# Performance work log

Measured on AMD Instinct MI355X. Metric: run time of the kernel, lower is better.

## Reference

```python
import jax, jax.numpy as jnp
import numpy as np

B, L1, L2 = 4, 1024, 512
D_PG, D_EX = 2304, 1024
H, HKV, DH = 8, 4, 256
SCALE = 256.0 ** -0.5


def _rope(x, cos, sin):
    # x: [B, L, h, DH]; cos/sin: [B, L, 1, DH//2]
    x = x.astype(jnp.float32)
    x1, x2 = jnp.split(x, 2, axis=-1)
    return jnp.concatenate([x1 * cos - x2 * sin, x2 * cos + x1 * sin], axis=-1)


def setup_inputs() -> dict:
    key = jax.random.key(0)
    ks = jax.random.split(key, 16)
    s = 0.02
    return {
        "pg_embeds": jax.random.normal(ks[0], (B, L1, D_PG), jnp.float32),
        "ex_embeds": jax.random.normal(ks[1], (B, L2, D_EX), jnp.float32),
        "cos": jax.random.normal(ks[2], (B, L1 + L2, 1, DH // 2), jnp.float32),
        "sin": jax.random.normal(ks[3], (B, L1 + L2, 1, DH // 2), jnp.float32),
        "attention_mask": jnp.zeros((B, L1 + L2, L1 + L2), jnp.float32),
        "Wq0": jax.random.normal(ks[4], (H * DH, D_PG), jnp.float32) * s,
        "Wk0": jax.random.normal(ks[5], (HKV * DH, D_PG), jnp.float32) * s,
        "Wv0": jax.random.normal(ks[6], (HKV * DH, D_PG), jnp.float32) * s,
        "Wo0": jax.random.normal(ks[7], (D_PG, H * DH), jnp.float32) * s,
        "Wq1": jax.random.normal(ks[8], (H * DH, D_EX), jnp.float32) * s,
        "Wk1": jax.random.normal(ks[9], (HKV * DH, D_EX), jnp.float32) * s,
        "Wv1": jax.random.normal(ks[10], (HKV * DH, D_EX), jnp.float32) * s,
        "Wo1": jax.random.normal(ks[11], (D_EX, H * DH), jnp.float32) * s,
    }


def reference(pg_embeds, ex_embeds, cos, sin, attention_mask,
              Wq0, Wk0, Wv0, Wo0, Wq1, Wk1, Wv1, Wo1):
    b, l1 = pg_embeds.shape[0], pg_embeds.shape[1]
    l2 = ex_embeds.shape[1]
    # per-stream QKV projections, then concat along sequence
    q = jnp.concatenate([
        (pg_embeds @ Wq0.T).reshape(b, l1, H, DH),
        (ex_embeds @ Wq1.T).reshape(b, l2, H, DH)], axis=1)
    k = jnp.concatenate([
        (pg_embeds @ Wk0.T).reshape(b, l1, HKV, DH),
        (ex_embeds @ Wk1.T).reshape(b, l2, HKV, DH)], axis=1)
    v = jnp.concatenate([
        (pg_embeds @ Wv0.T).reshape(b, l1, HKV, DH),
        (ex_embeds @ Wv1.T).reshape(b, l2, HKV, DH)], axis=1)
    q = _rope(q, cos, sin)  # fp32
    k = _rope(k, cos, sin)
    # GQA: repeat KV heads to match query heads
    rep = H // HKV
    k = jnp.repeat(k, rep, axis=2)
    v = jnp.repeat(jnp.repeat(v, rep, axis=2).astype(jnp.float32), 1, axis=0)
    # scores: [B, H, L, L]
    scores = jnp.einsum('bqhd,bkhd->bhqk', q, k) * SCALE
    scores = scores + attention_mask[:, None, :, :]
    p = jax.nn.softmax(scores, axis=-1)
    att = jnp.einsum('bhqk,bkhd->bqhd', p, v).reshape(b, l1 + l2, H * DH)
    out0 = att[:, :l1] @ Wo0.T
    out1 = att[:, l1:] @ Wo1.T
    return (out0, out1)
```

## Files before the change

### kernel.cpp

```cpp
#include <hip/hip_runtime.h>
#include <stdint.h>
#include <stddef.h>


typedef _Float16 f16;
typedef _Float16 f16x8 __attribute__((ext_vector_type(8)));
typedef _Float16 f16x4 __attribute__((ext_vector_type(4)));
typedef float    f32x4 __attribute__((ext_vector_type(4)));

__device__ __forceinline__ void async_ld16(const void* g, void* l) {
  __builtin_amdgcn_global_load_lds((const __attribute__((address_space(1))) void*)g,
                                   (__attribute__((address_space(3))) void*)l,
                                   16, 0, 0);
}

template <typename Epi>
__device__ __forceinline__ void gemm_core(f16* At, f16* Bt,
                                          const f16* __restrict__ A, int lda,
                                          const f16* __restrict__ Bm, int ldb,
                                          int K, Epi&& epi)
{
  const int t    = threadIdx.x;
  const int w    = t >> 6;
  const int lane = t & 63;
  const int q4   = lane >> 4;
  const int l16  = lane & 15;
  const int wm   = w >> 1;
  const int wn   = w & 1;

  const f32x4 vzero = {0.f, 0.f, 0.f, 0.f};
  f32x4 acc[4][4];
#pragma unroll
  for (int i = 0; i < 4; ++i)
#pragma unroll
    for (int j = 0; j < 4; ++j) acc[i][j] = vzero;

  const int srow = t >> 2;
  const int scol = (t & 3) << 3;
  const f16* aP = A  + (size_t)srow * lda + scol;
  const f16* bP = Bm + (size_t)srow * ldb + scol;
  f16* ldsA0 = At + w * 512;
  f16* ldsA1 = At + 2048 + w * 512;
  f16* ldsB0 = Bt + w * 512;
  f16* ldsB1 = Bt + 2048 + w * 512;
  const size_t a64 = (size_t)64 * lda;
  const size_t b64 = (size_t)64 * ldb;

  for (int k0 = 0; k0 < K; k0 += 32) {
    async_ld16(aP + k0,        ldsA0);
    async_ld16(aP + a64 + k0,  ldsA1);
    async_ld16(bP + k0,        ldsB0);
    async_ld16(bP + b64 + k0,  ldsB1);
    __syncthreads();

    f16x8 af[4], bf[4];
#pragma unroll
    for (int mi = 0; mi < 4; ++mi)
      af[mi] = *(const f16x8*)(At + (wm * 64 + mi * 16 + l16) * 32 + q4 * 8);
#pragma unroll
    for (int ni = 0; ni < 4; ++ni)
      bf[ni] = *(const f16x8*)(Bt + (wn * 64 + ni * 16 + l16) * 32 + q4 * 8);

#pragma unroll
    for (int mi = 0; mi < 4; ++mi)
#pragma unroll
      for (int ni = 0; ni < 4; ++ni)
        acc[mi][ni] = __builtin_amdgcn_mfma_f32_16x16x32_f16(af[mi], bf[ni], acc[mi][ni], 0, 0, 0);
    __syncthreads();
  }

#pragma unroll
  for (int mi = 0; mi < 4; ++mi)
#pragma unroll
    for (int ni = 0; ni < 4; ++ni)
#pragma unroll
      for (int r = 0; r < 4; ++r)
        epi(wm * 64 + mi * 16 + q4 * 4 + r, wn * 64 + ni * 16 + l16, acc[mi][ni][r]);
}

__global__ __launch_bounds__(256) void k_qkv(
    const f16* __restrict__ xpg, const f16* __restrict__ xex,
    const f16* __restrict__ W0,  const f16* __restrict__ W1,
    const float* __restrict__ cs, const float* __restrict__ sn,
    f16* __restrict__ q, f16* __restrict__ k, f16* __restrict__ v)
{
  __shared__ alignas(16) f16 At[128 * 32];
  __shared__ alignas(16) f16 Bt[128 * 32];
  const int idx = blockIdx.x;
  const bool s0 = idx < 1024;
  int by, bx, K;
  const f16 *A, *B;
  if (s0) { by = idx >> 5; bx = idx & 31; K = 2304;
            A = xpg + (size_t)by * 128 * 2304; B = W0 + (size_t)bx * 128 * 2304; }
  else    { int j = idx - 1024; by = j >> 5; bx = j & 31; K = 1024;
            A = xex + (size_t)by * 128 * 1024; B = W1 + (size_t)bx * 128 * 1024; }
  const int rowbase = by * 128, colbase = bx * 128;
  gemm_core(At, Bt, A, K, B, K, K, [&](int r, int c, float fv) {
    int m = rowbase + r;
    int row = s0 ? ((m >> 10) * 1536 + (m & 1023))
                 : ((m >> 9) * 1536 + 1024 + (m & 511));
    int col = colbase + c;
    float p = __shfl_xor(fv, 1, 64);
    if (col < 3072) {
      int j = (col & 255) >> 1;
      float cv = cs[(size_t)row * 128 + j];
      float sv = sn[(size_t)row * 128 + j];
      float y = (col & 1) ? (fv * cv + p * sv) : (fv * cv - p * sv);
      f16 h = (f16)y;
      if (col < 2048) q[(size_t)row * 2048 + col]        = h;
      else            k[(size_t)row * 1024 + col - 2048] = h;
    } else {
      v[(size_t)row * 1024 + col - 3072] = (f16)fv;
    }
  });
}

__global__ __launch_bounds__(256) void k_vtrans(const f16* __restrict__ v,
                                                f16* __restrict__ vt)
{
  __shared__ f16 tile[32][33];
  const int b = blockIdx.z;
  const int d0 = blockIdx.x * 32, l0 = blockIdx.y * 32;
  const int t = threadIdx.x;
  const int tr = t >> 5, tc = t & 31;
#pragma unroll
  for (int i = 0; i < 4; ++i) {
    int l = l0 + tr + i * 8;
    tile[tr + i * 8][tc] = v[((size_t)b * 1536 + l) * 1024 + d0 + tc];
  }
  __syncthreads();
#pragma unroll
  for (int i = 0; i < 4; ++i) {
    int d = d0 + tr + i * 8;
    int g = d >> 8, dw = d & 255;
    vt[(((size_t)b * 4 + g) * 256 + dw) * 1536 + l0 + tc] = tile[tc][tr + i * 8];
  }
}

__global__ __launch_bounds__(256) void k_attn(
    const f16* __restrict__ qb, const f16* __restrict__ kb,
    const f16* __restrict__ mask, f16* __restrict__ Sdst,
    const f16* __restrict__ Psrc, const f16* __restrict__ vt,
    f16* __restrict__ att0, f16* __restrict__ att1,
    int b_sc, int b_pv, int npv)
{
  __shared__ alignas(16) f16 At[128 * 32];
  __shared__ alignas(16) f16 Bt[128 * 32];
  const int idx = blockIdx.x;
  if (idx < npv) {
    const int h = idx / 24, rem = idx % 24, by = rem >> 1, bx = rem & 1;
    const f16* A = Psrc + (size_t)h * 1536 * 1536 + (size_t)by * 128 * 1536;
    const f16* B = vt + (size_t)(b_pv * 4 + (h >> 1)) * 256 * 1536 + (size_t)bx * 128 * 1536;
    const int rowbase = by * 128, colbase = bx * 128;
    gemm_core(At, Bt, A, 1536, B, 1536, 1536, [&](int r, int c, float fv) {
      int m = rowbase + r;
      if (m < 1024) att0[((size_t)(b_pv * 1024 + m))       * 2048 + h * 256 + colbase + c] = (f16)fv;
      else          att1[((size_t)(b_pv * 512 + m - 1024)) * 2048 + h * 256 + colbase + c] = (f16)fv;
    });
  } else {
    const int j = idx - npv;
    const int h = j / 144, rem = j % 144, by = rem / 12, bx = rem % 12;
    const f16* A = qb + (size_t)b_sc * 1536 * 2048 + h * 256 + (size_t)by * 128 * 2048;
    const f16* B = kb + (size_t)b_sc * 1536 * 1024 + (h >> 1) * 256 + (size_t)bx * 128 * 1024;
    f16* Sz = Sdst + (size_t)h * 1536 * 1536;
    const f16* mb = mask + (size_t)b_sc * 1536 * 1536;
    const int rowbase = by * 128, colbase = bx * 128;
    gemm_core(At, Bt, A, 2048, B, 1024, 256, [&](int r, int c, float fv) {
      size_t i = (size_t)(rowbase + r) * 1536 + colbase + c;
      Sz[i] = (f16)(fv * 0.0625f + (float)mb[i]);
    });
  }
}

__global__ __launch_bounds__(256) void k_softmax(f16* __restrict__ S)
{
  const int row = blockIdx.x * 4 + (threadIdx.x >> 6);
  const int lane = threadIdx.x & 63;
  f16* p = S + (size_t)row * 1536 + lane * 8;
  f16x8 v0 = *(const f16x8*)p;
  f16x8 v1 = *(const f16x8*)(p + 512);
  f16x8 v2 = *(const f16x8*)(p + 1024);
  float x[24];
#pragma unroll
  for (int i = 0; i < 8; ++i) {
    x[i] = (float)v0[i]; x[8 + i] = (float)v1[i]; x[16 + i] = (float)v2[i];
  }
  float mx = x[0];
#pragma unroll
  for (int i = 1; i < 24; ++i) mx = fmaxf(mx, x[i]);
#pragma unroll
  for (int o = 32; o > 0; o >>= 1) mx = fmaxf(mx, __shfl_xor(mx, o, 64));
  float s = 0.f;
#pragma unroll
  for (int i = 0; i < 24; ++i) { x[i] = __expf(x[i] - mx); s += x[i]; }
#pragma unroll
  for (int o = 32; o > 0; o >>= 1) s += __shfl_xor(s, o, 64);
  const float inv = 1.f / s;
  f16x8 o0, o1, o2;
#pragma unroll
  for (int i = 0; i < 8; ++i) {
    o0[i] = (f16)(x[i] * inv); o1[i] = (f16)(x[8 + i] * inv); o2[i] = (f16)(x[16 + i] * inv);
  }
  *(f16x8*)p = o0; *(f16x8*)(p + 512) = o1; *(f16x8*)(p + 1024) = o2;
}

__global__ __launch_bounds__(256) void k_tail(
    const f16* __restrict__ Psrc, const f16* __restrict__ vt,
    f16* __restrict__ att0, f16* __restrict__ att1,
    const f16* __restrict__ wo0, const f16* __restrict__ wo1,
    float* __restrict__ out0, float* __restrict__ out1)
{
  __shared__ alignas(16) f16 At[128 * 32];
  __shared__ alignas(16) f16 Bt[128 * 32];
  const int idx = blockIdx.x;
  if (idx < 192) {
    const int h = idx / 24, rem = idx % 24, by = rem >> 1, bx = rem & 1;
    const f16* A = Psrc + (size_t)h * 1536 * 1536 + (size_t)by * 128 * 1536;
    const f16* B = vt + (size_t)(3 * 4 + (h >> 1)) * 256 * 1536 + (size_t)bx * 128 * 1536;
    const int rowbase = by * 128, colbase = bx * 128;
    gemm_core(At, Bt, A, 1536, B, 1536, 1536, [&](int r, int c, float fv) {
      int m = rowbase + r;
      if (m < 1024) att0[((size_t)(3 * 1024 + m))       * 2048 + h * 256 + colbase + c] = (f16)fv;
      else          att1[((size_t)(3 * 512 + m - 1024)) * 2048 + h * 256 + colbase + c] = (f16)fv;
    });
  } else if (idx < 624) {
    const int j = idx - 192;
    const int by = j / 18, bx = j % 18;
    const f16* A = att0 + (size_t)by * 128 * 2048;
    const f16* B = wo0 + (size_t)bx * 128 * 2048;
    const int rowbase = by * 128, colbase = bx * 128;
    gemm_core(At, Bt, A, 2048, B, 2048, 2048, [&](int r, int c, float fv) {
      out0[(size_t)(rowbase + r) * 2304 + colbase + c] = fv;
    });
  } else {
    const int j = idx - 624;
    const int by = j >> 3, bx = j & 7;
    const f16* A = att1 + (size_t)by * 128 * 2048;
    const f16* B = wo1 + (size_t)bx * 128 * 2048;
    const int rowbase = by * 128, colbase = bx * 128;
    gemm_core(At, Bt, A, 2048, B, 2048, 2048, [&](int r, int c, float fv) {
      out1[(size_t)(rowbase + r) * 1024 + colbase + c] = fv;
    });
  }
}

__global__ __launch_bounds__(256) void k_oproj3(
    const f16* __restrict__ att0, const f16* __restrict__ att1,
    const f16* __restrict__ wo0,  const f16* __restrict__ wo1,
    float* __restrict__ out0, float* __restrict__ out1)
{
  __shared__ alignas(16) f16 At[128 * 32];
  __shared__ alignas(16) f16 Bt[128 * 32];
  const int idx = blockIdx.x;
  int by, bx, ldc;
  const f16 *A, *B;
  float* C;
  if (idx < 144) { by = 24 + idx / 18; bx = idx % 18;
                   A = att0 + (size_t)by * 128 * 2048; B = wo0 + (size_t)bx * 128 * 2048;
                   C = out0; ldc = 2304; }
  else           { int j = idx - 144; by = 12 + (j >> 3); bx = j & 7;
                   A = att1 + (size_t)by * 128 * 2048; B = wo1 + (size_t)bx * 128 * 2048;
                   C = out1; ldc = 1024; }
  const int rowbase = by * 128, colbase = bx * 128;
  gemm_core(At, Bt, A, 2048, B, 2048, 2048, [&](int r, int c, float fv) {
    C[(size_t)(rowbase + r) * ldc + colbase + c] = fv;
  });
}

__global__ __launch_bounds__(256) void k_cast_all(
    const float* __restrict__ s0, const float* __restrict__ s1,
    const float* __restrict__ s2, const float* __restrict__ s3,
    const float* __restrict__ s4, const float* __restrict__ s5,
    f16* __restrict__ ws)
{
  const size_t gid = ((size_t)blockIdx.x * 256 + threadIdx.x) * 4;
  const float* s; size_t off, dst;
  if      (gid < 9437184ull)  { s = s0; off = gid;               dst = 0ull        + off; }
  else if (gid < 11534336ull) { s = s1; off = gid - 9437184ull;  dst = 9437184ull  + off; }
  else if (gid < 13893632ull) { s = s2; off = gid - 11534336ull; dst = 18612224ull + off; }
  else if (gid < 18612224ull) { s = s3; off = gid - 13893632ull; dst = 20971520ull + off; }
  else if (gid < 19660800ull) { s = s4; off = gid - 18612224ull; dst = 28835840ull + off; }
  else                        { s = s5; off = gid - 19660800ull; dst = 29884416ull + off; }
  float4 v = *(const float4*)(s + off);
  f16x4 o = {(f16)v.x, (f16)v.y, (f16)v.z, (f16)v.w};
  *(f16x4*)(ws + dst) = o;
}

__global__ __launch_bounds__(256) void k_cast_wr(
    const float* __restrict__ wq0, const float* __restrict__ wk0,
    const float* __restrict__ wq1, const float* __restrict__ wk1,
    f16* __restrict__ W0c, f16* __restrict__ W1c)
{
  const int idx = blockIdx.x;
  const float* src; f16* dstm; int K, r, drow;
  if      (idx < 2048) { src = wq0; dstm = W0c; K = 2304; r = idx;        drow = idx; }
  else if (idx < 3072) { src = wk0; dstm = W0c; K = 2304; r = idx - 2048; drow = idx; }
  else if (idx < 5120) { src = wq1; dstm = W1c; K = 1024; r = idx - 3072; drow = idx - 3072; }
  else                 { src = wk1; dstm = W1c; K = 1024; r = idx - 5120; drow = idx - 3072; }
  const int w = r & 255;
  const int srow = (r & ~255) + (w >> 1) + ((w & 1) << 7);
  const float* sp = src + (size_t)srow * K;
  f16* dp = dstm + (size_t)drow * K;
  for (int c = threadIdx.x * 4; c < K; c += 1024) {
    float4 v = *(const float4*)(sp + c);
    f16x4 o = {(f16)v.x, (f16)v.y, (f16)v.z, (f16)v.w};
    *(f16x4*)(dp + c) = o;
  }
}

__global__ __launch_bounds__(256) void k_cast_mask(const float* __restrict__ m,
                                                   f16* __restrict__ mh)
{
  const size_t gid = ((size_t)blockIdx.x * 256 + threadIdx.x) * 4;
  float4 v = *(const float4*)(m + gid);
  f16x4 o = {(f16)v.x, (f16)v.y, (f16)v.z, (f16)v.w};
  *(f16x4*)(mh + gid) = o;
}

extern "C" void kernel_launch(void* const* d_in, const int* in_sizes, int n_in,
                              void* d_out, int out_size, void* d_ws, size_t ws_size,
                              hipStream_t stream)
{
  (void)in_sizes; (void)n_in; (void)out_size; (void)ws_size;
  const float* pg  = (const float*)d_in[0];
  const float* ex  = (const float*)d_in[1];
  const float* cs  = (const float*)d_in[2];
  const float* sn  = (const float*)d_in[3];
  const float* msk = (const float*)d_in[4];

  char* ws = (char*)d_ws;
  f16* xpg  = (f16*)(ws + 0);
  f16* xex  = (f16*)(ws + 18874368);
  f16* W0c  = (f16*)(ws + 23068672);
  f16* wo0c = (f16*)(ws + 41943040);
  f16* W1c  = (f16*)(ws + 51380224);
  f16* wo1c = (f16*)(ws + 59768832);
  f16* qb   = (f16*)(ws + 63963136);
  f16* kb   = (f16*)(ws + 89128960);
  f16* vb   = (f16*)(ws + 101711872);
  f16* vt   = (f16*)(ws + 114294784);
  f16* att0 = (f16*)(ws + 126877696);
  f16* att1 = (f16*)(ws + 143654912);
  f16* S0   = (f16*)(ws + 152043520);
  f16* S1   = (f16*)(ws + 189792256);
  f16* mkh  = W0c;
  float* out0 = (float*)d_out;
  float* out1 = out0 + 9437184;

  k_cast_all<<<21248, 256, 0, stream>>>(
      pg, ex, (const float*)d_in[7], (const float*)d_in[8],
      (const float*)d_in[11], (const float*)d_in[12], (f16*)ws);
  k_cast_wr<<<6144, 256, 0, stream>>>(
      (const float*)d_in[5], (const float*)d_in[6],
      (const float*)d_in[9], (const float*)d_in[10], W0c, W1c);

  k_qkv<<<1536, 256, 0, stream>>>(xpg, xex, W0c, W1c, cs, sn, qb, kb, vb);

  k_cast_mask<<<9216, 256, 0, stream>>>(msk, mkh);
  k_vtrans<<<dim3(32, 48, 4), 256, 0, stream>>>(vb, vt);

  k_attn<<<1152, 256, 0, stream>>>(qb, kb, mkh, S0, S0, vt, att0, att1, 0, 0, 0);
  k_softmax<<<3072, 256, 0, stream>>>(S0);
  k_attn<<<1344, 256, 0, stream>>>(qb, kb, mkh, S1, S0, vt, att0, att1, 1, 0, 192);
  k_softmax<<<3072, 256, 0, stream>>>(S1);
  k_attn<<<1344, 256, 0, stream>>>(qb, kb, mkh, S0, S1, vt, att0, att1, 2, 1, 192);
  k_softmax<<<3072, 256, 0, stream>>>(S0);
  k_attn<<<1344, 256, 0, stream>>>(qb, kb, mkh, S1, S0, vt, att0, att1, 3, 2, 192);
  k_softmax<<<3072, 256, 0, stream>>>(S1);

  k_tail<<<720, 256, 0, stream>>>(S1, vt, att0, att1, wo0c, wo1c, out0, out1);
  k_oproj3<<<176, 256, 0, stream>>>(att0, att1, wo0c, wo1c, out0, out1);
}
```

Before: 719.6 us.

## Move RoPE out of QKV epilogue, merge prep kernels, overlap output projection with attention

```diff
diff --git a/kernel.cpp b/kernel.cpp
--- a/kernel.cpp
+++ b/kernel.cpp
@@ -81,7 +81,6 @@
 __global__ __launch_bounds__(256) void k_qkv(
     const f16* __restrict__ xpg, const f16* __restrict__ xex,
     const f16* __restrict__ W0,  const f16* __restrict__ W1,
-    const float* __restrict__ cs, const float* __restrict__ sn,
     f16* __restrict__ q, f16* __restrict__ k, f16* __restrict__ v)
 {
   __shared__ alignas(16) f16 At[128 * 32];
@@ -100,40 +99,59 @@
     int row = s0 ? ((m >> 10) * 1536 + (m & 1023))
                  : ((m >> 9) * 1536 + 1024 + (m & 511));
     int col = colbase + c;
-    float p = __shfl_xor(fv, 1, 64);
-    if (col < 3072) {
-      int j = (col & 255) >> 1;
-      float cv = cs[(size_t)row * 128 + j];
-      float sv = sn[(size_t)row * 128 + j];
-      float y = (col & 1) ? (fv * cv + p * sv) : (fv * cv - p * sv);
-      f16 h = (f16)y;
-      if (col < 2048) q[(size_t)row * 2048 + col]        = h;
-      else            k[(size_t)row * 1024 + col - 2048] = h;
-    } else {
-      v[(size_t)row * 1024 + col - 3072] = (f16)fv;
+    f16 h = (f16)fv;
+    if      (col < 2048) q[(size_t)row * 2048 + col]        = h;
+    else if (col < 3072) k[(size_t)row * 1024 + col - 2048] = h;
+    else                 v[(size_t)row * 1024 + col - 3072] = h;
+  });
+}
+
+__global__ __launch_bounds__(256) void k_post(
+    f16* __restrict__ q, f16* __restrict__ k,
+    const float* __restrict__ cs, const float* __restrict__ sn,
+    const float* __restrict__ msk, f16* __restrict__ mkh,
+    const f16* __restrict__ v, f16* __restrict__ vt)
+{
+  const int blk = blockIdx.x;
+  if (blk < 6144) {
+    __shared__ f16 tile[32][33];
+    const int b = blk / 1536, r0 = blk % 1536;
+    const int d0 = (r0 & 31) * 32, l0 = (r0 >> 5) * 32;
+    const int t = threadIdx.x;
+    const int tr = t >> 5, tc = t & 31;
+#pragma unroll
+    for (int i = 0; i < 4; ++i)
+      tile[tr + i * 8][tc] = v[((size_t)b * 1536 + l0 + tr + i * 8) * 1024 + d0 + tc];
+    __syncthreads();
+#pragma unroll
+    for (int i = 0; i < 4; ++i) {
+      int d = d0 + tr + i * 8;
+      vt[(((size_t)b * 4 + (d >> 8)) * 256 + (d & 255)) * 1536 + l0 + tc] = tile[tc][tr + i * 8];
     }
-  });
-}
-
-__global__ __launch_bounds__(256) void k_vtrans(const f16* __restrict__ v,
-                                                f16* __restrict__ vt)
-{
-  __shared__ f16 tile[32][33];
-  const int b = blockIdx.z;
-  const int d0 = blockIdx.x * 32, l0 = blockIdx.y * 32;
-  const int t = threadIdx.x;
-  const int tr = t >> 5, tc = t & 31;
-#pragma unroll
-  for (int i = 0; i < 4; ++i) {
-    int l = l0 + tr + i * 8;
-    tile[tr + i * 8][tc] = v[((size_t)b * 1536 + l) * 1024 + d0 + tc];
-  }
-  __syncthreads();
-#pragma unroll
-  for (int i = 0; i < 4; ++i) {
-    int d = d0 + tr + i * 8;
-    int g = d >> 8, dw = d & 255;
-    vt[(((size_t)b * 4 + g) * 256 + dw) * 1536 + l0 + tc] = tile[tc][tr + i * 8];
+  } else if (blk < 15360) {
+    const size_t gid = ((size_t)(blk - 6144) * 256 + threadIdx.x) * 4;
+    float4 m4 = *(const float4*)(msk + gid);
+    f16x4 o = {(f16)m4.x, (f16)m4.y, (f16)m4.z, (f16)m4.w};
+    *(f16x4*)(mkh + gid) = o;
+  } else {
+    const size_t tid8 = ((size_t)(blk - 15360) * 256 + threadIdx.x) * 8;
+    f16* base; size_t row; int col;
+    if (tid8 < 12582912ull) { base = q + tid8; row = tid8 >> 11; col = (int)(tid8 & 2047); }
+    else { size_t f = tid8 - 12582912ull; base = k + f; row = f >> 10; col = (int)(f & 1023); }
+    const int j0 = (col & 255) >> 1;
+    f16x8 x = *(const f16x8*)base;
+    float4 c4 = *(const float4*)(cs + row * 128 + j0);
+    float4 s4 = *(const float4*)(sn + row * 128 + j0);
+    f16x8 o;
+    const float cc[4] = {c4.x, c4.y, c4.z, c4.w};
+    const float ss[4] = {s4.x, s4.y, s4.z, s4.w};
+#pragma unroll
+    for (int p = 0; p < 4; ++p) {
+      float x1 = (float)x[2 * p], x2 = (float)x[2 * p + 1];
+      o[2 * p]     = (f16)(x1 * cc[p] - x2 * ss[p]);
+      o[2 * p + 1] = (f16)(x2 * cc[p] + x1 * ss[p]);
+    }
+    *(f16x8*)base = o;
   }
 }
 
@@ -142,13 +160,28 @@
     const f16* __restrict__ mask, f16* __restrict__ Sdst,
     const f16* __restrict__ Psrc, const f16* __restrict__ vt,
     f16* __restrict__ att0, f16* __restrict__ att1,
-    int b_sc, int b_pv, int npv)
+    const f16* __restrict__ wo0, const f16* __restrict__ wo1,
+    float* __restrict__ out0, float* __restrict__ out1,
+    int b_sc, int b_pv, int b_op, int npv, int nop)
 {
   __shared__ alignas(16) f16 At[128 * 32];
   __shared__ alignas(16) f16 Bt[128 * 32];
   const int idx = blockIdx.x;
-  if (idx < npv) {
-    const int h = idx / 24, rem = idx % 24, by = rem >> 1, bx = rem & 1;
+  if (idx < nop) {
+    int by, bx, ldc; const f16 *A, *B; float* C;
+    if (idx < 144) { by = b_op * 8 + idx / 18; bx = idx % 18;
+                     A = att0 + (size_t)by * 128 * 2048; B = wo0 + (size_t)bx * 128 * 2048;
+                     C = out0; ldc = 2304; }
+    else           { int j = idx - 144; by = b_op * 4 + (j >> 3); bx = j & 7;
+                     A = att1 + (size_t)by * 128 * 2048; B = wo1 + (size_t)bx * 128 * 2048;
+                     C = out1; ldc = 1024; }
+    const int rowbase = by * 128, colbase = bx * 128;
+    gemm_core(At, Bt, A, 2048, B, 2048, 2048, [&](int r, int c, float fv) {
+      C[(size_t)(rowbase + r) * ldc + colbase + c] = fv;
+    });
+  } else if (idx < nop + npv) {
+    const int j = idx - nop;
+    const int h = j / 24, rem = j % 24, by = rem >> 1, bx = rem & 1;
     const f16* A = Psrc + (size_t)h * 1536 * 1536 + (size_t)by * 128 * 1536;
     const f16* B = vt + (size_t)(b_pv * 4 + (h >> 1)) * 256 * 1536 + (size_t)bx * 128 * 1536;
     const int rowbase = by * 128, colbase = bx * 128;
@@ -158,7 +191,7 @@
       else          att1[((size_t)(b_pv * 512 + m - 1024)) * 2048 + h * 256 + colbase + c] = (f16)fv;
     });
   } else {
-    const int j = idx - npv;
+    const int j = idx - nop - npv;
     const int h = j / 144, rem = j % 144, by = rem / 12, bx = rem % 12;
     const f16* A = qb + (size_t)b_sc * 1536 * 2048 + h * 256 + (size_t)by * 128 * 2048;
     const f16* B = kb + (size_t)b_sc * 1536 * 1024 + (h >> 1) * 256 + (size_t)bx * 128 * 1024;
@@ -202,69 +235,6 @@
     o0[i] = (f16)(x[i] * inv); o1[i] = (f16)(x[8 + i] * inv); o2[i] = (f16)(x[16 + i] * inv);
   }
   *(f16x8*)p = o0; *(f16x8*)(p + 512) = o1; *(f16x8*)(p + 1024) = o2;
-}
-
-__global__ __launch_bounds__(256) void k_tail(
-    const f16* __restrict__ Psrc, const f16* __restrict__ vt,
-    f16* __restrict__ att0, f16* __restrict__ att1,
-    const f16* __restrict__ wo0, const f16* __restrict__ wo1,
-    float* __restrict__ out0, float* __restrict__ out1)
-{
-  __shared__ alignas(16) f16 At[128 * 32];
-  __shared__ alignas(16) f16 Bt[128 * 32];
-  const int idx = blockIdx.x;
-  if (idx < 192) {
-    const int h = idx / 24, rem = idx % 24, by = rem >> 1, bx = rem & 1;
-    const f16* A = Psrc + (size_t)h * 1536 * 1536 + (size_t)by * 128 * 1536;
-    const f16* B = vt + (size_t)(3 * 4 + (h >> 1)) * 256 * 1536 + (size_t)bx * 128 * 1536;
-    const int rowbase = by * 128, colbase = bx * 128;
-    gemm_core(At, Bt, A, 1536, B, 1536, 1536, [&](int r, int c, float fv) {
-      int m = rowbase + r;
-      if (m < 1024) att0[((size_t)(3 * 1024 + m))       * 2048 + h * 256 + colbase + c] = (f16)fv;
-      else          att1[((size_t)(3 * 512 + m - 1024)) * 2048 + h * 256 + colbase + c] = (f16)fv;
-    });
-  } else if (idx < 624) {
-    const int j = idx - 192;
-    const int by = j / 18, bx = j % 18;
-    const f16* A = att0 + (size_t)by * 128 * 2048;
-    const f16* B = wo0 + (size_t)bx * 128 * 2048;
-    const int rowbase = by * 128, colbase = bx * 128;
-    gemm_core(At, Bt, A, 2048, B, 2048, 2048, [&](int r, int c, float fv) {
-      out0[(size_t)(rowbase + r) * 2304 + colbase + c] = fv;
-    });
-  } else {
-    const int j = idx - 624;
-    const int by = j >> 3, bx = j & 7;
-    const f16* A = att1 + (size_t)by * 128 * 2048;
-    const f16* B = wo1 + (size_t)bx * 128 * 2048;
-    const int rowbase = by * 128, colbase = bx * 128;
-    gemm_core(At, Bt, A, 2048, B, 2048, 2048, [&](int r, int c, float fv) {
-      out1[(size_t)(rowbase + r) * 1024 + colbase + c] = fv;
-    });
-  }
-}
-
-__global__ __launch_bounds__(256) void k_oproj3(
-    const f16* __restrict__ att0, const f16* __restrict__ att1,
-    const f16* __restrict__ wo0,  const f16* __restrict__ wo1,
-    float* __restrict__ out0, float* __restrict__ out1)
-{
-  __shared__ alignas(16) f16 At[128 * 32];
-  __shared__ alignas(16) f16 Bt[128 * 32];
-  const int idx = blockIdx.x;
-  int by, bx, ldc;
-  const f16 *A, *B;
-  float* C;
-  if (idx < 144) { by = 24 + idx / 18; bx = idx % 18;
-                   A = att0 + (size_t)by * 128 * 2048; B = wo0 + (size_t)bx * 128 * 2048;
-                   C = out0; ldc = 2304; }
-  else           { int j = idx - 144; by = 12 + (j >> 3); bx = j & 7;
-                   A = att1 + (size_t)by * 128 * 2048; B = wo1 + (size_t)bx * 128 * 2048;
-                   C = out1; ldc = 1024; }
-  const int rowbase = by * 128, colbase = bx * 128;
-  gemm_core(At, Bt, A, 2048, B, 2048, 2048, [&](int r, int c, float fv) {
-    C[(size_t)(rowbase + r) * ldc + colbase + c] = fv;
-  });
 }
 
 __global__ __launch_bounds__(256) void k_cast_all(
@@ -306,15 +276,6 @@
     f16x4 o = {(f16)v.x, (f16)v.y, (f16)v.z, (f16)v.w};
     *(f16x4*)(dp + c) = o;
   }
-}
-
-__global__ __launch_bounds__(256) void k_cast_mask(const float* __restrict__ m,
-                                                   f16* __restrict__ mh)
-{
-  const size_t gid = ((size_t)blockIdx.x * 256 + threadIdx.x) * 4;
-  float4 v = *(const float4*)(m + gid);
-  f16x4 o = {(f16)v.x, (f16)v.y, (f16)v.z, (f16)v.w};
-  *(f16x4*)(mh + gid) = o;
 }
 
 extern "C" void kernel_launch(void* const* d_in, const int* in_sizes, int n_in,
@@ -354,20 +315,19 @@
       (const float*)d_in[5], (const float*)d_in[6],
       (const float*)d_in[9], (const float*)d_in[10], W0c, W1c);
 
-  k_qkv<<<1536, 256, 0, stream>>>(xpg, xex, W0c, W1c, cs, sn, qb, kb, vb);
-
-  k_cast_mask<<<9216, 256, 0, stream>>>(msk, mkh);
-  k_vtrans<<<dim3(32, 48, 4), 256, 0, stream>>>(vb, vt);
-
-  k_attn<<<1152, 256, 0, stream>>>(qb, kb, mkh, S0, S0, vt, att0, att1, 0, 0, 0);
+  k_qkv<<<1536, 256, 0, stream>>>(xpg, xex, W0c, W1c, qb, kb, vb);
+
+  k_post<<<24576, 256, 0, stream>>>(qb, kb, cs, sn, msk, mkh, vb, vt);
+
+  k_attn<<<1152, 256, 0, stream>>>(qb, kb, mkh, S0, S0, vt, att0, att1, wo0c, wo1c, out0, out1, 0, 0, 0, 0, 0);
   k_softmax<<<3072, 256, 0, stream>>>(S0);
-  k_attn<<<1344, 256, 0, stream>>>(qb, kb, mkh, S1, S0, vt, att0, att1, 1, 0, 192);
+  k_attn<<<1344, 256, 0, stream>>>(qb, kb, mkh, S1, S0, vt, att0, att1, wo0c, wo1c, out0, out1, 1, 0, 0, 192, 0);
   k_softmax<<<3072, 256, 0, stream>>>(S1);
-  k_attn<<<1344, 256, 0, stream>>>(qb, kb, mkh, S0, S1, vt, att0, att1, 2, 1, 192);
+  k_attn<<<1520, 256, 0, stream>>>(qb, kb, mkh, S0, S1, vt, att0, att1, wo0c, wo1c, out0, out1, 2, 1, 0, 192, 176);
   k_softmax<<<3072, 256, 0, stream>>>(S0);
-  k_attn<<<1344, 256, 0, stream>>>(qb, kb, mkh, S1, S0, vt, att0, att1, 3, 2, 192);
+  k_attn<<<1520, 256, 0, stream>>>(qb, kb, mkh, S1, S0, vt, att0, att1, wo0c, wo1c, out0, out1, 3, 2, 1, 192, 176);
   k_softmax<<<3072, 256, 0, stream>>>(S1);
 
-  k_tail<<<720, 256, 0, stream>>>(S1, vt, att0, att1, wo0c, wo1c, out0, out1);
-  k_oproj3<<<176, 256, 0, stream>>>(att0, att1, wo0c, wo1c, out0, out1);
-}
+  k_attn<<<368, 256, 0, stream>>>(qb, kb, mkh, S0, S1, vt, att0, att1, wo0c, wo1c, out0, out1, 0, 3, 2, 192, 176);
+  k_attn<<<176, 256, 0, stream>>>(qb, kb, mkh, S0, S1, vt, att0, att1, wo0c, wo1c, out0, out1, 0, 0, 3, 0, 176);
+}
```

After: 690.9 us. 4.0% less time.
